# Optimization experiments

Measured on AMD Instinct MI355X. Metric: run time of the kernel, lower is better.

The kernel has to match this reference:

```python
import jax, jax.numpy as jnp
import numpy as np

B, N, D, L, H, DH, M, FF = 4, 2048, 512, 6, 8, 64, 266, 2048
EPS_LN = 1e-5
KERNEL_EPS = 1e-4


def fixed_pos_emb(n, dim):
    # performer_pytorch FixedPositionalEmbedding: cat(sin, cos) over half-dims
    inv_freq = 1.0 / (10000.0 ** (jnp.arange(0, dim, 2, dtype=jnp.float32) / dim))
    t = jnp.arange(n, dtype=jnp.float32)
    s = jnp.einsum('i,j->ij', t, inv_freq)  # [n, dim//2]
    return jnp.concatenate([jnp.sin(s), jnp.cos(s)], axis=-1)  # [n, dim]


def layer_norm(x, g, b):
    mu = x.mean(-1, keepdims=True)
    var = ((x - mu) ** 2).mean(-1, keepdims=True)
    return (x - mu) * jax.lax.rsqrt(var + EPS_LN) * g + b


def rotate_every_two(t):
    t1 = t[..., ::2]
    t2 = t[..., 1::2]
    return jnp.stack([-t2, t1], axis=-1).reshape(t.shape)


def apply_rotary(q, k, sinu):
    # sinu: [n, DH] = cat(sin_half, cos_half); repeat each value twice (interleaved)
    half = sinu.shape[-1] // 2
    sin = jnp.repeat(sinu[:, :half], 2, axis=-1)  # [n, DH]
    cos = jnp.repeat(sinu[:, half:], 2, axis=-1)
    q = q * cos + rotate_every_two(q) * sin
    k = k * cos + rotate_every_two(k) * sin
    return q, k


def softmax_kernel(data, proj, is_query):
    # data: [B,H,N,DH], proj: [M,DH]
    d = data.shape[-1]
    data_normalizer = d ** -0.25
    ratio = proj.shape[0] ** -0.5
    data_dash = jnp.einsum('bhnd,md->bhnm', data * data_normalizer, proj)
    diag = (data ** 2).sum(-1) * 0.5 * (data_normalizer ** 2)  # [B,H,N]
    if is_query:
        m = jnp.max(data_dash, axis=-1, keepdims=True)
    else:
        m = jnp.max(data_dash)
    return ratio * (jnp.exp(data_dash - diag[..., None] - m) + KERNEL_EPS)


def linear_attention(qf, kf, v):
    # qf/kf: [B,H,N,M], v: [B,H,N,DH]  (non-causal FAVOR+)
    k_sum = kf.sum(axis=-2)  # [B,H,M]
    d_inv = 1.0 / jnp.einsum('bhnm,bhm->bhn', qf, k_sum)
    context = jnp.einsum('bhnm,bhne->bhme', kf, v)  # [B,H,M,DH]
    return jnp.einsum('bhme,bhnm,bhn->bhne', context, qf, d_inv)


def setup_inputs() -> dict:
    key = jax.random.key(0)
    ks = jax.random.split(key, 8)
    std = 0.02
    inp = {
        'x': jax.random.normal(ks[0], (B, N, D), jnp.float32),
        'Wq': jax.random.normal(ks[1], (L, D, H * DH), jnp.float32) * std,
        'Wk': jax.random.normal(ks[2], (L, D, H * DH), jnp.float32) * std,
        'Wv': jax.random.normal(ks[3], (L, D, H * DH), jnp.float32) * std,
        'Wo': jax.random.normal(ks[4], (L, H * DH, D), jnp.float32) * std,
        'proj': jax.random.normal(ks[5], (L, M, DH), jnp.float32),
        'ln1_g': jnp.ones((L, D), jnp.float32),
        'ln1_b': jnp.zeros((L, D), jnp.float32),
        'W1': jax.random.normal(ks[6], (L, D, FF), jnp.float32) * std,
        'b1': jnp.zeros((L, FF), jnp.float32),
        'W2': jax.random.normal(ks[7], (L, FF, D), jnp.float32) * std,
        'b2': jnp.zeros((L, D), jnp.float32),
        'ln2_g': jnp.ones((L, D), jnp.float32),
        'ln2_b': jnp.zeros((L, D), jnp.float32),
        'lnf_g': jnp.ones((D,), jnp.float32),
        'lnf_b': jnp.zeros((D,), jnp.float32),
    }
    return inp


def reference(x, Wq, Wk, Wv, Wo, proj, ln1_g, ln1_b, W1, b1, W2, b2, ln2_g, ln2_b, lnf_g, lnf_b):
    n = x.shape[1]
    x = x + fixed_pos_emb(n, D)[None]          # additive sinusoidal emb
    sinu = fixed_pos_emb(n, DH)                 # per-head rotary table [n, DH]
    for i in range(L):
        # --- PreLayerNorm FAVOR+ self-attention ---
        h = layer_norm(x, ln1_g[i], ln1_b[i])
        q = jnp.einsum('bnd,de->bne', h, Wq[i]).reshape(B, n, H, DH).transpose(0, 2, 1, 3)
        k = jnp.einsum('bnd,de->bne', h, Wk[i]).reshape(B, n, H, DH).transpose(0, 2, 1, 3)
        v = jnp.einsum('bnd,de->bne', h, Wv[i]).reshape(B, n, H, DH).transpose(0, 2, 1, 3)
        q, k = apply_rotary(q, k, sinu)
        qf = softmax_kernel(q, proj[i], True)
        kf = softmax_kernel(k, proj[i], False)
        o = linear_attention(qf, kf, v)         # [B,H,n,DH]
        o = o.transpose(0, 2, 1, 3).reshape(B, n, H * DH)
        x = x + jnp.einsum('bne,ed->bnd', o, Wo[i])
        # --- PreLayerNorm FFN (GELU) ---
        h = layer_norm(x, ln2_g[i], ln2_b[i])
        h = jax.nn.gelu(jnp.einsum('bnd,df->bnf', h, W1[i]) + b1[i], approximate=False)
        x = x + jnp.einsum('bnf,fd->bnd', h, W2[i]) + b2[i]
    return layer_norm(x, lnf_g, lnf_b)
```

## Files before the change

kernel.cpp:

```cpp
#include <hip/hip_runtime.h>
#include <hip/hip_bf16.h>
#include <cstdint>

typedef float v4f __attribute__((ext_vector_type(4)));
typedef short v8s __attribute__((ext_vector_type(8)));
typedef unsigned short u16;

#define N_SEQ 2048
#define D_MODEL 512
#define N_LAYER 6
#define N_HEAD 8
#define D_HEAD 64
#define M_FEAT 266
#define M_PAD 288
#define M_ALLOC 384
#define FF_DIM 2048
#define BATCH 4
#define ROWS 8192
#define BHN 65536

__device__ __forceinline__ float b2f(u16 u) {
  return __uint_as_float(((uint32_t)u) << 16);
}
__device__ __forceinline__ u16 f2b(float f) {
  union { __hip_bfloat16 h; u16 u; } c;
  c.h = __float2bfloat16(f);
  return c.u;
}
__device__ __forceinline__ float wave_sum(float v) {
#pragma unroll
  for (int o = 1; o < 64; o <<= 1) v += __shfl_xor(v, o);
  return v;
}
__device__ __forceinline__ float wave_max(float v) {
#pragma unroll
  for (int o = 1; o < 64; o <<= 1) v = fmaxf(v, __shfl_xor(v, o));
  return v;
}

__device__ __forceinline__ float gelu_f(float x) {
  float ax = fabsf(x) * 0.70710678118f;
  float tt = __builtin_amdgcn_rcpf(fmaf(0.3275911f, ax, 1.0f));
  float poly = tt * fmaf(tt, fmaf(tt, fmaf(tt, fmaf(tt, 1.061405429f, -1.453152027f),
                                           1.421413741f), -0.284496736f), 0.254829592f);
  float er = 1.0f - poly * __expf(-ax * ax);
  er = copysignf(er, x);
  return 0.5f * x * (1.0f + er);
}

__device__ __forceinline__ void mfma_bf16(v4f& d, v8s a, v8s b) {
  asm volatile("v_mfma_f32_16x16x32_bf16 %0, %1, %2, %0" : "+v"(d) : "v"(a), "v"(b));
}

__device__ __forceinline__ void async16(const u16* g, u16* l) {
  __builtin_amdgcn_global_load_lds(
      (const __attribute__((address_space(1))) uint32_t*)g,
      (__attribute__((address_space(3))) uint32_t*)l, 16, 0, 0);
}

template <int EPI, int KSPLIT>
__global__ void __launch_bounds__(512, 2)
gemm3s(const u16* __restrict__ A, const u16* __restrict__ B,
       void* __restrict__ Cv, const float* __restrict__ bias,
       int K, int ldc)
{
  extern __shared__ u16 lds[];
  const int t = threadIdx.x;
  const int lane = t & 63;
  const int w = t >> 6;
  const int wm = w >> 2;
  const int wn = w & 3;
  const int tiM = blockIdx.x << 7, tiN = blockIdx.y << 8;
  const int ks = (KSPLIT > 1) ? blockIdx.z : 0;
  const int kchunk = K / KSPLIT;
  const int NT = kchunk >> 6;

  const int rr = lane & 15;
  const int kq = (lane >> 4) << 3;
  const int swz = (rr & 7) << 3;
  const int c0 = kq ^ swz;
  const int c1 = (32 + kq) ^ swz;

  const int prow = t >> 3;
  const int scol = (((t & 7) ^ (prow & 7)) << 3);
  const u16* Abase = A + (long long)(tiM + prow) * K + scol + (long long)ks * kchunk;
  const u16* Bbase = B + (long long)(tiN + prow) * K + scol + (long long)ks * kchunk;
  const long long r64 = 64LL * K;

  v4f acc[4][4] = {};

  auto stage6 = [&](int s, int kt) {
    const u16* sa = Abase + (long long)kt * 64;
    u16* da = &lds[s * 24576 + t * 8];
    async16(sa, da);
    async16(sa + r64, da + 4096);
    const u16* sb = Bbase + (long long)kt * 64;
    u16* db = &lds[s * 24576 + 8192 + t * 8];
#pragma unroll
    for (int j = 0; j < 4; j++) async16(sb + (long long)j * r64, db + j * 4096);
  };

  stage6(0, 0);
  stage6(1, 1);
  asm volatile("s_waitcnt vmcnt(6)" ::: "memory");
  __builtin_amdgcn_s_barrier();

  for (int kt = 0; kt < NT; ++kt) {
    const int s = kt % 3;
    const int sp = (kt + 2) % 3;
    const bool st = (kt + 2 < NT);
    const int ab = s * 24576;
    const int bb = ab + 8192;
    v8s a0[4], a1[4], b0[4], b1[4];
#pragma unroll
    for (int i = 0; i < 4; i++) {
      a0[i] = *(const v8s*)&lds[ab + (wm * 64 + i * 16 + rr) * 64 + c0];
      a1[i] = *(const v8s*)&lds[ab + (wm * 64 + i * 16 + rr) * 64 + c1];
      b0[i] = *(const v8s*)&lds[bb + (wn * 64 + i * 16 + rr) * 64 + c0];
      b1[i] = *(const v8s*)&lds[bb + (wn * 64 + i * 16 + rr) * 64 + c1];
    }
    if (st) stage6(sp, kt + 2);
    __builtin_amdgcn_s_setprio(1);
#pragma unroll
    for (int m = 0; m < 4; m++)
#pragma unroll
      for (int n = 0; n < 4; n++) {
        mfma_bf16(acc[m][n], a0[m], b0[n]);
        mfma_bf16(acc[m][n], a1[m], b1[n]);
      }
    __builtin_amdgcn_s_setprio(0);
    if (st) asm volatile("s_waitcnt vmcnt(6)" ::: "memory");
    else    asm volatile("s_waitcnt vmcnt(0)" ::: "memory");
    __builtin_amdgcn_s_barrier();
  }

  __builtin_amdgcn_sched_barrier(0);
  asm volatile("s_nop 7\ns_nop 7\ns_nop 7");
  __builtin_amdgcn_sched_barrier(0);

  const int r4 = (lane >> 4) << 2;
  const int cc = lane & 15;
#pragma unroll
  for (int mf = 0; mf < 4; mf++)
#pragma unroll
    for (int nf = 0; nf < 4; nf++)
#pragma unroll
      for (int i = 0; i < 4; i++) {
        int row = tiM + wm * 64 + mf * 16 + r4 + i;
        int col = tiN + wn * 64 + nf * 16 + cc;
        float v = acc[mf][nf][i];
        if (EPI == 0) {
          ((u16*)Cv)[(long long)row * ldc + col] = f2b(v);
        } else if (EPI == 3) {
          ((u16*)Cv)[(long long)row * ldc + col] = f2b(gelu_f(v + bias[col]));
        } else {
          ((float*)Cv)[((long long)ks * ROWS + row) * ldc + col] = v;
        }
      }
}

__global__ void ff2red(const float* __restrict__ part, const float* __restrict__ bias,
                       float* __restrict__ x)
{
  long long i = ((long long)blockIdx.x * 256 + threadIdx.x) * 8;
  int col = (int)(i & 511);
  v4f s0 = {}, s1 = {};
#pragma unroll
  for (int ks = 0; ks < 2; ks++) {
    const float* p = part + (long long)ks * (ROWS * 512LL) + i;
    s0 += *(const v4f*)p;
    s1 += *(const v4f*)(p + 4);
  }
  v4f b0 = *(const v4f*)(bias + col);
  v4f b1 = *(const v4f*)(bias + col + 4);
  v4f x0 = *(const v4f*)(x + i), x1 = *(const v4f*)(x + i + 4);
  x0 += s0 + b0;
  x1 += s1 + b1;
  *(v4f*)(x + i) = x0;
  *(v4f*)(x + i + 4) = x1;
}

template <int EPI, int BN, int KSPLIT>
__global__ void __launch_bounds__(256, 4)
gemm2(const u16* __restrict__ A, const u16* __restrict__ B,
      void* __restrict__ Cv, const float* __restrict__ bias,
      int K, int ldc, long long sA, long long sB, long long sC,
      float scale, int Ncap, int Mcap, unsigned int* __restrict__ gmax)
{
  __shared__ u16 As[2][128 * 32];
  __shared__ u16 Bs[2][BN * 32];
  __shared__ float smax[4];
  const int zz = blockIdx.z;
  const int z = (KSPLIT > 1) ? zz / KSPLIT : zz;
  const int ks = (KSPLIT > 1) ? zz % KSPLIT : 0;
  const int kchunk = K / KSPLIT;
  const u16* Ag = A + (long long)z * sA + ks * kchunk;
  const u16* Bg = B + (long long)z * sB + ks * kchunk;
  const int t = threadIdx.x;
  const int lane = t & 63;
  const int w = t >> 6;
  constexpr int NF = BN / 32;
  const int wm = (w >> 1) << 6;
  const int wn = (w & 1) * (BN / 2);
  const int tiM = blockIdx.x << 7, tiN = blockIdx.y * BN;

  const int srow = t >> 2;
  const int scol = (t & 3) << 3;
  const u16* Ap = Ag + (long long)(tiM + srow) * K + scol;
  const u16* Bp = Bg + (long long)(tiN + srow) * K + scol;
  const long long rstride = 64LL * K;

  const int rr = lane & 15;
  const int kc = (lane >> 4) << 3;

  v4f acc[4][NF] = {};

  const int nk = kchunk >> 5;
  auto stage = [&](int buf, int k0) {
    async16(Ap + k0, &As[buf][t * 8]);
    async16(Ap + k0 + rstride, &As[buf][t * 8 + 2048]);
    async16(Bp + k0, &Bs[buf][t * 8]);
    if (BN == 128) async16(Bp + k0 + rstride, &Bs[buf][t * 8 + 2048]);
  };

  stage(0, 0);
  __syncthreads();
  int cur = 0;
  for (int kt = 0; kt < nk; ++kt) {
    if (kt + 1 < nk) stage(cur ^ 1, (kt + 1) << 5);
    v8s af[4], bf[NF];
#pragma unroll
    for (int i = 0; i < 4; i++) af[i] = *(const v8s*)&As[cur][(wm + rr + i * 16) * 32 + kc];
#pragma unroll
    for (int i = 0; i < NF; i++) bf[i] = *(const v8s*)&Bs[cur][(wn + rr + i * 16) * 32 + kc];
#pragma unroll
    for (int fm = 0; fm < 4; fm++)
#pragma unroll
      for (int fn = 0; fn < NF; fn++)
        mfma_bf16(acc[fm][fn], af[fm], bf[fn]);
    __syncthreads();
    cur ^= 1;
  }

  __builtin_amdgcn_sched_barrier(0);
  asm volatile("s_nop 7\ns_nop 7\ns_nop 7");
  __builtin_amdgcn_sched_barrier(0);

  const int r4 = (lane >> 4) << 2;
  const int cc = lane & 15;
  float lmax = -3e38f;
#pragma unroll
  for (int fm = 0; fm < 4; fm++)
#pragma unroll
    for (int fn = 0; fn < NF; fn++)
#pragma unroll
      for (int i = 0; i < 4; i++) {
        int row = tiM + wm + fm * 16 + r4 + i;
        int col = tiN + wn + fn * 16 + cc;
        float v = acc[fm][fn][i];
        if (EPI == 5) {
          if (row < Mcap && col < Ncap)
            ((float*)Cv)[((long long)zz * M_ALLOC + row) * 64 + col] = v;
        } else if (EPI == 6) {
          float sv = v * scale;
          if (col < Ncap) ((float*)Cv)[(long long)row * ldc + col] = sv;
          if (col < M_FEAT) lmax = fmaxf(lmax, sv);
        }
      }

  if (EPI == 6) {
    lmax = wave_max(lmax);
    if (lane == 0) smax[w] = lmax;
    __syncthreads();
    if (t == 0) {
      float m = fmaxf(fmaxf(smax[0], smax[1]), fmaxf(smax[2], smax[3]));
      unsigned int u = __float_as_uint(m);
      unsigned int key = (u & 0x80000000u) ? ~u : (u | 0x80000000u);
      atomicMax(gmax, key);
    }
  }
}

template <int EPI>
__global__ void __launch_bounds__(256, 6)
gemm_small(const u16* __restrict__ A, const u16* __restrict__ B,
           void* __restrict__ Cv, const float* __restrict__ bias,
           int K, int ldc, long long sA, long long sB)
{
  __shared__ u16 As[2][64 * 32];
  __shared__ u16 Bs[2][64 * 32];
  const int z = blockIdx.z;
  const u16* Ag = A + (long long)z * sA;
  const u16* Bg = B + (long long)z * sB;
  const int t = threadIdx.x;
  const int lane = t & 63;
  const int w = t >> 6;
  const int wm = (w >> 1) << 5;
  const int wn = (w & 1) << 5;
  const int tiM = blockIdx.x << 6, tiN = blockIdx.y << 6;

  const int srow = t >> 2;
  const int scol = (t & 3) << 3;
  const u16* Ap = Ag + (long long)(tiM + srow) * K + scol;
  const u16* Bp = Bg + (long long)(tiN + srow) * K + scol;

  const int rr = lane & 15;
  const int kc = (lane >> 4) << 3;

  v4f acc[2][2] = {};

  const int nk = K >> 5;
  auto stage = [&](int buf, int k0) {
    async16(Ap + k0, &As[buf][t * 8]);
    async16(Bp + k0, &Bs[buf][t * 8]);
  };

  stage(0, 0);
  __syncthreads();
  int cur = 0;
  for (int kt = 0; kt < nk; ++kt) {
    if (kt + 1 < nk) stage(cur ^ 1, (kt + 1) << 5);
    v8s af[2], bf[2];
#pragma unroll
    for (int i = 0; i < 2; i++) af[i] = *(const v8s*)&As[cur][(wm + rr + i * 16) * 32 + kc];
#pragma unroll
    for (int i = 0; i < 2; i++) bf[i] = *(const v8s*)&Bs[cur][(wn + rr + i * 16) * 32 + kc];
#pragma unroll
    for (int fm = 0; fm < 2; fm++)
#pragma unroll
      for (int fn = 0; fn < 2; fn++)
        mfma_bf16(acc[fm][fn], af[fm], bf[fn]);
    __syncthreads();
    cur ^= 1;
  }

  __builtin_amdgcn_sched_barrier(0);
  asm volatile("s_nop 7\ns_nop 7\ns_nop 7");
  __builtin_amdgcn_sched_barrier(0);

  const int r4 = (lane >> 4) << 2;
  const int cc = lane & 15;
#pragma unroll
  for (int fm = 0; fm < 2; fm++)
#pragma unroll
    for (int fn = 0; fn < 2; fn++)
#pragma unroll
      for (int i = 0; i < 4; i++) {
        int row = tiM + wm + fm * 16 + r4 + i;
        int col = tiN + wn + fn * 16 + cc;
        float v = acc[fm][fn][i];
        if (EPI == 0) {
          ((u16*)Cv)[(long long)row * ldc + col] = f2b(v);
        } else if (EPI == 2) {
          long long idx = (long long)row * ldc + col;
          float bb = bias ? bias[col] : 0.0f;
          ((float*)Cv)[idx] += v + bb;
        } else if (EPI == 3) {
          ((u16*)Cv)[(long long)row * ldc + col] = f2b(gelu_f(v + bias[col]));
        } else {
          int b_ = z >> 3, h_ = z & 7;
          ((u16*)Cv)[(long long)(b_ * N_SEQ + row) * 512 + h_ * 64 + col] = f2b(v);
        }
      }
}

__global__ void __launch_bounds__(384, 3)
ddq_qf(const u16* __restrict__ qr, const u16* __restrict__ proj,
       const float* __restrict__ diag, const float* __restrict__ ksum,
       u16* __restrict__ qf)
{
  __shared__ u16 As[2][64 * 32];
  __shared__ u16 Bs[2][288 * 32];
  __shared__ float redw[6][64];
  __shared__ float rowv[64];
  __shared__ float sdg[64];
  const int bh = blockIdx.z;
  const int tiM = blockIdx.x << 6;
  const int t = threadIdx.x;
  const int lane = t & 63;
  const int w = t >> 6;
  const u16* Ag = qr + (long long)bh * (N_SEQ * 64);
  const int srow = t >> 2, scol = (t & 3) << 3;
  const u16* Ap = Ag + (long long)(tiM + srow) * 64 + scol;
  const int rr = lane & 15, kc = (lane >> 4) << 3;
  const int wn = w * 48;

  if (t < 64) sdg[t] = diag[(long long)bh * N_SEQ + tiM + t];

  v4f acc[4][3] = {};
  auto stage = [&](int buf, int k0) {
    if (t < 256) async16(Ap + k0, &As[buf][t * 8]);
#pragma unroll
    for (int j = 0; j < 3; j++) {
      int idx = j * 384 + t;
      async16(proj + (long long)(idx >> 2) * 64 + ((idx & 3) << 3) + k0,
              &Bs[buf][j * 3072 + t * 8]);
    }
  };

  stage(0, 0);
  __syncthreads();
  for (int kt = 0; kt < 2; ++kt) {
    if (kt == 0) stage(1, 32);
    v8s af[4], bf[3];
#pragma unroll
    for (int i = 0; i < 4; i++) af[i] = *(const v8s*)&As[kt][(rr + i * 16) * 32 + kc];
#pragma unroll
    for (int i = 0; i < 3; i++) bf[i] = *(const v8s*)&Bs[kt][(wn + i * 16 + rr) * 32 + kc];
#pragma unroll
    for (int fm = 0; fm < 4; fm++)
#pragma unroll
      for (int fn = 0; fn < 3; fn++)
        mfma_bf16(acc[fm][fn], af[fm], bf[fn]);
    __syncthreads();
  }

  __builtin_amdgcn_sched_barrier(0);
  asm volatile("s_nop 7\ns_nop 7\ns_nop 7");
  __builtin_amdgcn_sched_barrier(0);

  const int r4 = (lane >> 4) << 2;
  const int cc = lane & 15;
  const float sc = 0.35355339f;

#pragma unroll
  for (int fm = 0; fm < 4; fm++)
#pragma unroll
    for (int i = 0; i < 4; i++) {
      float m = -3e38f;
#pragma unroll
      for (int fn = 0; fn < 3; fn++) {
        int col = wn + fn * 16 + cc;
        float v = acc[fm][fn][i] * sc;
        if (col < M_FEAT) m = fmaxf(m, v);
      }
#pragma unroll
      for (int o = 1; o < 16; o <<= 1) m = fmaxf(m, __shfl_xor(m, o));
      if (cc == 0) redw[w][fm * 16 + r4 + i] = m;
    }
  __syncthreads();
  if (t < 64) {
    float g = redw[0][t];
#pragma unroll
    for (int ww = 1; ww < 6; ww++) g = fmaxf(g, redw[ww][t]);
    rowv[t] = g;
  }
  __syncthreads();

  float ksv[3];
#pragma unroll
  for (int fn = 0; fn < 3; fn++) ksv[fn] = ksum[bh * M_PAD + wn + fn * 16 + cc];

#pragma unroll
  for (int fm = 0; fm < 4; fm++)
#pragma unroll
    for (int i = 0; i < 4; i++) {
      int row = fm * 16 + r4 + i;
      float gm = rowv[row];
      float dg = sdg[row];
      float s = 0.0f;
#pragma unroll
      for (int fn = 0; fn < 3; fn++) {
        float e = 0.06131389f * (expf(acc[fm][fn][i] * sc - dg - gm) + 1e-4f);
        acc[fm][fn][i] = e;
        s += e * ksv[fn];
      }
#pragma unroll
      for (int o = 1; o < 16; o <<= 1) s += __shfl_xor(s, o);
      if (cc == 0) redw[w][row] = s;
    }
  __syncthreads();
  if (t < 64) {
    float s = redw[0][t];
#pragma unroll
    for (int ww = 1; ww < 6; ww++) s += redw[ww][t];
    rowv[t] = 1.0f / s;
  }
  __syncthreads();

#pragma unroll
  for (int fm = 0; fm < 4; fm++)
#pragma unroll
    for (int i = 0; i < 4; i++) {
      int row = fm * 16 + r4 + i;
      float dinv = rowv[row];
#pragma unroll
      for (int fn = 0; fn < 3; fn++) {
        int col = wn + fn * 16 + cc;
        qf[((long long)bh * N_SEQ + tiM + row) * M_PAD + col] =
            f2b(acc[fm][fn][i] * dinv);
      }
    }
}

template <bool F32OUT>
__global__ void ln_kernel(const float* __restrict__ x, const float* __restrict__ g,
                          const float* __restrict__ b, void* __restrict__ out)
{
  const int row = blockIdx.x * 4 + (threadIdx.x >> 6);
  const int lane = threadIdx.x & 63;
  const float* xr = x + (long long)row * D_MODEL + lane * 8;
  v4f v0 = *(const v4f*)xr;
  v4f v1 = *(const v4f*)(xr + 4);
  float s = v0[0] + v0[1] + v0[2] + v0[3] + v1[0] + v1[1] + v1[2] + v1[3];
  float sq = v0[0]*v0[0] + v0[1]*v0[1] + v0[2]*v0[2] + v0[3]*v0[3]
           + v1[0]*v1[0] + v1[1]*v1[1] + v1[2]*v1[2] + v1[3]*v1[3];
  s = wave_sum(s);
  sq = wave_sum(sq);
  float mu = s * (1.0f / D_MODEL);
  float var = sq * (1.0f / D_MODEL) - mu * mu;
  float rstd = rsqrtf(var + 1e-5f);
  v4f g0 = *(const v4f*)(g + lane * 8), g1 = *(const v4f*)(g + lane * 8 + 4);
  v4f bb0 = *(const v4f*)(b + lane * 8), bb1 = *(const v4f*)(b + lane * 8 + 4);
  float y[8];
#pragma unroll
  for (int j = 0; j < 4; j++) y[j] = (v0[j] - mu) * rstd * g0[j] + bb0[j];
#pragma unroll
  for (int j = 0; j < 4; j++) y[4 + j] = (v1[j] - mu) * rstd * g1[j] + bb1[j];
  if (F32OUT) {
    float* op = (float*)out + (long long)row * D_MODEL + lane * 8;
    v4f o0 = {y[0], y[1], y[2], y[3]}, o1 = {y[4], y[5], y[6], y[7]};
    *(v4f*)op = o0;
    *(v4f*)(op + 4) = o1;
  } else {
    u16* op = (u16*)out + (long long)row * D_MODEL + lane * 8;
    alignas(16) u16 tmp[8];
#pragma unroll
    for (int j = 0; j < 8; j++) tmp[j] = f2b(y[j]);
    *(v8s*)op = *(v8s*)tmp;
  }
}

__global__ void posadd(const float* __restrict__ xin, float* __restrict__ x)
{
  long long i = (long long)blockIdx.x * 256 + threadIdx.x;
  int d = (int)(i & 511);
  int n = (int)((i >> 9) & 2047);
  int j = d & 255;
  float sarg = (float)n * expf(-0.035977892f * (float)j);
  float pe = (d < 256) ? sinf(sarg) : cosf(sarg);
  x[i] = xin[i] + pe;
}

__global__ void rotab(float* __restrict__ ts, float* __restrict__ tc)
{
  int i = blockIdx.x * 64 + threadIdx.x;
  int n = i >> 5, j = i & 31;
  float sarg = (float)n * expf(-0.28782314f * (float)j);
  float s, c;
  sincosf(sarg, &s, &c);
  ts[i] = s;
  tc[i] = c;
}

__global__ void rotary_kernel(const u16* __restrict__ qkv,
                              const float* __restrict__ ts, const float* __restrict__ tc,
                              u16* __restrict__ qr, u16* __restrict__ kr,
                              float* __restrict__ dq, float* __restrict__ dk)
{
  int bid = blockIdx.x * 4 + (threadIdx.x >> 6);
  int n = bid & 2047;
  int h = (bid >> 11) & 7;
  int b = bid >> 14;
  int lane = threadIdx.x & 63;
  long long src = ((long long)(b * N_SEQ + n)) * 1536 + h * 64 + lane;
  float qv = b2f(qkv[src]);
  float kv = b2f(qkv[src + 512]);
  int j = lane >> 1;
  float sn = ts[n * 32 + j], cn = tc[n * 32 + j];
  float qp = __shfl_xor(qv, 1), kp = __shfl_xor(kv, 1);
  float qrv = (lane & 1) ? (qv * cn + qp * sn) : (qv * cn - qp * sn);
  float krv = (lane & 1) ? (kv * cn + kp * sn) : (kv * cn - kp * sn);
  u16 qb = f2b(qrv), kb = f2b(krv);
  long long dst = ((long long)bid) * 64 + lane;
  qr[dst] = qb;
  kr[dst] = kb;
  float q2 = b2f(qb); q2 *= q2;
  float k2 = b2f(kb); k2 *= k2;
  q2 = wave_sum(q2);
  k2 = wave_sum(k2);
  if (lane == 0) { dq[bid] = q2 * 0.0625f; dk[bid] = k2 * 0.0625f; }
}

__global__ void vtrans(const u16* __restrict__ qkv, u16* __restrict__ vT)
{
  int bid = blockIdx.x;
  int nt = bid & 31;
  int h = (bid >> 5) & 7;
  int b = bid >> 8;
  __shared__ u16 st[64][72];
  int t = threadIdx.x;
  int r = t >> 2, c = (t & 3) << 4;
  long long src = ((long long)(b * N_SEQ + nt * 64 + r)) * 1536 + 1024 + h * 64 + c;
  *(v8s*)&st[r][c] = *(const v8s*)(qkv + src);
  *(v8s*)&st[r][c + 8] = *(const v8s*)(qkv + src + 8);
  __syncthreads();
  alignas(16) u16 tmp[16];
#pragma unroll
  for (int jj = 0; jj < 16; jj++) tmp[jj] = st[c + jj][r];
  long long dst = ((long long)((b * 8 + h) * 64 + r)) * N_SEQ + nt * 64 + c;
  *(v8s*)(vT + dst) = *(v8s*)&tmp[0];
  *(v8s*)(vT + dst + 8) = *(v8s*)&tmp[8];
}

__global__ void wtrans(const float* __restrict__ src, u16* __restrict__ dst,
                       int Ks, int Ns, long long sSrc, long long sDst)
{
  int l = blockIdx.z;
  src += (long long)l * sSrc;
  dst += (long long)l * sDst;
  int n0 = blockIdx.x << 6, k0 = blockIdx.y << 6;
  __shared__ float st[64][68];
  int t = threadIdx.x;
  int r = t >> 2, c = (t & 3) << 4;
  const float* sp = src + (long long)(k0 + r) * Ns + n0 + c;
#pragma unroll
  for (int jj = 0; jj < 16; jj += 4) *(v4f*)&st[r][c + jj] = *(const v4f*)(sp + jj);
  __syncthreads();
  alignas(16) u16 tmp[16];
#pragma unroll
  for (int jj = 0; jj < 16; jj++) tmp[jj] = f2b(st[c + jj][r]);
  u16* dp = dst + (long long)(n0 + r) * Ks + k0 + c;
  *(v8s*)(dp) = *(v8s*)&tmp[0];
  *(v8s*)(dp + 8) = *(v8s*)&tmp[8];
}

__global__ void projconv(const float* __restrict__ proj, u16* __restrict__ out)
{
  int i = blockIdx.x * 256 + threadIdx.x;
  int dh = i & 63;
  int m = (i >> 6) % M_ALLOC;
  int l = i / (M_ALLOC * 64);
  float v = (m < M_FEAT) ? proj[((long long)l * M_FEAT + m) * 64 + dh] : 0.0f;
  out[i] = f2b(v);
}

__global__ void resetmax(unsigned int* p) { *p = 0u; }

__global__ void kfprep(const float* __restrict__ dd, const float* __restrict__ diag,
                       const unsigned int* __restrict__ kmax,
                       u16* __restrict__ kfT, float* __restrict__ part)
{
  int ntile = blockIdx.x;
  int m0 = blockIdx.y << 6;
  int bh = blockIdx.z;
  int n0 = ntile << 6;
  __shared__ float st[64][65];
  unsigned int kk = kmax[0];
  float km = (kk & 0x80000000u) ? __uint_as_float(kk ^ 0x80000000u)
                                : __uint_as_float(~kk);
  int t = threadIdx.x;
  int r = t >> 2, c = (t & 3) << 4;
  const float* dp = dd + ((long long)bh * N_SEQ + n0 + r) * M_PAD + m0 + c;
  float dg = diag[(long long)bh * N_SEQ + n0 + r];
  float vals[16];
  if (m0 + c + 16 <= M_PAD) {
#pragma unroll
    for (int j = 0; j < 16; j += 4) *(v4f*)&vals[j] = *(const v4f*)(dp + j);
  } else {
#pragma unroll
    for (int j = 0; j < 16; j++) vals[j] = (m0 + c + j < M_PAD) ? dp[j] : 0.0f;
  }
#pragma unroll
  for (int j = 0; j < 16; j++) {
    int m = m0 + c + j;
    float e = (m < M_FEAT) ? 0.06131389f * (expf(vals[j] - dg - km) + 1e-4f) : 0.0f;
    st[r][c + j] = e;
  }
  __syncthreads();
  int mr = t >> 2, nc = (t & 3) << 4;
  float s = 0.0f;
  alignas(16) u16 tmp[16];
#pragma unroll
  for (int j = 0; j < 16; j++) {
    float e = st[nc + j][mr];
    s += e;
    tmp[j] = f2b(e);
  }
  s += __shfl_xor(s, 1);
  s += __shfl_xor(s, 2);
  int m = m0 + mr;
  if (m < M_PAD) {
    u16* op = kfT + ((long long)bh * M_ALLOC + m) * N_SEQ + n0 + nc;
    *(v8s*)op = *(v8s*)&tmp[0];
    *(v8s*)(op + 8) = *(v8s*)&tmp[8];
    if ((t & 3) == 0)
      part[((long long)bh * M_PAD + m) * 32 + ntile] = s;
  }
}

__global__ void ksumred(const float* __restrict__ part, float* __restrict__ ksum)
{
  int i = blockIdx.x * 256 + threadIdx.x;
  if (i >= 32 * M_PAD) return;
  const float* p = part + (long long)i * 32;
  float s = 0.0f;
#pragma unroll
  for (int j = 0; j < 32; j += 4) {
    v4f v = *(const v4f*)(p + j);
    s += v[0] + v[1] + v[2] + v[3];
  }
  ksum[i] = s;
}

__global__ void ctxred(const float* __restrict__ part, u16* __restrict__ ctxT)
{
  int bh = blockIdx.y;
  int m0 = blockIdx.x << 6;
  __shared__ float st[64][65];
  int t = threadIdx.x;
  int r = t >> 2, c = (t & 3) << 4;
  int m = m0 + r;
  v4f s[4] = {};
  if (m < M_PAD) {
    for (int ks = 0; ks < 8; ks++) {
      const float* p = part + (((long long)bh * 8 + ks) * M_ALLOC + m) * 64 + c;
#pragma unroll
      for (int j = 0; j < 4; j++) s[j] += *(const v4f*)(p + j * 4);
    }
  }
#pragma unroll
  for (int j = 0; j < 4; j++)
#pragma unroll
    for (int e = 0; e < 4; e++) st[r][c + j * 4 + e] = s[j][e];
  __syncthreads();
  int e = t >> 2, mc = (t & 3) << 4;
  if (m0 + mc < M_PAD) {
    alignas(16) u16 tmp[16];
#pragma unroll
    for (int j = 0; j < 16; j++) tmp[j] = f2b(st[mc + j][e]);
    u16* op = ctxT + ((long long)bh * 64 + e) * M_PAD + m0 + mc;
    *(v8s*)op = *(v8s*)&tmp[0];
    *(v8s*)(op + 8) = *(v8s*)&tmp[8];
  }
}

extern "C" void kernel_launch(void* const* d_in, const int* in_sizes, int n_in,
                              void* d_out, int out_size, void* d_ws, size_t ws_size,
                              hipStream_t stream)
{
  const float* x_in = (const float*)d_in[0];
  const float* Wq  = (const float*)d_in[1];
  const float* Wk  = (const float*)d_in[2];
  const float* Wv  = (const float*)d_in[3];
  const float* Wo  = (const float*)d_in[4];
  const float* Pr  = (const float*)d_in[5];
  const float* ln1g = (const float*)d_in[6];
  const float* ln1b = (const float*)d_in[7];
  const float* W1  = (const float*)d_in[8];
  const float* b1  = (const float*)d_in[9];
  const float* W2  = (const float*)d_in[10];
  const float* b2  = (const float*)d_in[11];
  const float* ln2g = (const float*)d_in[12];
  const float* ln2b = (const float*)d_in[13];
  const float* lnfg = (const float*)d_in[14];
  const float* lnfb = (const float*)d_in[15];

  hipFuncSetAttribute(reinterpret_cast<const void*>(&gemm3s<0, 1>),
                      hipFuncAttributeMaxDynamicSharedMemorySize, 147456);
  hipFuncSetAttribute(reinterpret_cast<const void*>(&gemm3s<3, 1>),
                      hipFuncAttributeMaxDynamicSharedMemorySize, 147456);
  hipFuncSetAttribute(reinterpret_cast<const void*>(&gemm3s<5, 2>),
                      hipFuncAttributeMaxDynamicSharedMemorySize, 147456);

  char* ws = (char*)d_ws;
  size_t off = 0;
  auto alloc = [&](size_t bytes) -> void* {
    void* p = ws + off;
    off = (off + bytes + 255) & ~(size_t)255;
    return p;
  };

  float* x      = (float*)alloc((size_t)ROWS * D_MODEL * 4);
  float* tsin   = (float*)alloc((size_t)N_SEQ * 32 * 4);
  float* tcos   = (float*)alloc((size_t)N_SEQ * 32 * 4);
  u16*   wqkvT  = (u16*)alloc((size_t)N_LAYER * 1536 * 512 * 2);
  u16*   woT    = (u16*)alloc((size_t)N_LAYER * 512 * 512 * 2);
  u16*   w1T    = (u16*)alloc((size_t)N_LAYER * 2048 * 512 * 2);
  u16*   w2T    = (u16*)alloc((size_t)N_LAYER * 512 * 2048 * 2);
  u16*   projT  = (u16*)alloc((size_t)N_LAYER * M_ALLOC * 64 * 2);
  u16*   hbuf   = (u16*)alloc((size_t)ROWS * D_MODEL * 2);
  u16*   obuf   = (u16*)alloc((size_t)ROWS * D_MODEL * 2);
  float* big    = (float*)alloc((size_t)32 * N_SEQ * M_PAD * 4);
  u16*   qrbuf  = (u16*)alloc((size_t)BHN * 64 * 2);
  u16*   krbuf  = (u16*)alloc((size_t)BHN * 64 * 2);
  u16*   vTbuf  = (u16*)alloc((size_t)BHN * 64 * 2);
  float* diagq  = (float*)alloc((size_t)BHN * 4);
  float* diagk  = (float*)alloc((size_t)BHN * 4);
  unsigned int* kmaxu = (unsigned int*)alloc(256);
  u16*   kfT    = (u16*)alloc((size_t)32 * M_ALLOC * N_SEQ * 2);
  float* part   = (float*)alloc((size_t)32 * 8 * M_ALLOC * 64 * 4);
  float* kspart = (float*)alloc((size_t)32 * M_PAD * 32 * 4);
  u16*   ctxT   = (u16*)alloc((size_t)32 * 64 * M_PAD * 2);
  float* ksum   = (float*)alloc((size_t)32 * M_PAD * 4);
  (void)alloc(1 << 20);
  (void)ws_size; (void)in_sizes; (void)n_in; (void)out_size;
  float* ff2part = (float*)kfT;

  posadd<<<16384, 256, 0, stream>>>(x_in, x);
  rotab<<<1024, 64, 0, stream>>>(tsin, tcos);
  wtrans<<<dim3(8, 8, 6), 256, 0, stream>>>(Wq, wqkvT, 512, 512, 512LL * 512, 1536LL * 512);
  wtrans<<<dim3(8, 8, 6), 256, 0, stream>>>(Wk, wqkvT + 512LL * 512, 512, 512, 512LL * 512, 1536LL * 512);
  wtrans<<<dim3(8, 8, 6), 256, 0, stream>>>(Wv, wqkvT + 1024LL * 512, 512, 512, 512LL * 512, 1536LL * 512);
  wtrans<<<dim3(8, 8, 6), 256, 0, stream>>>(Wo, woT, 512, 512, 512LL * 512, 512LL * 512);
  wtrans<<<dim3(32, 8, 6), 256, 0, stream>>>(W1, w1T, 512, 2048, 512LL * 2048, 2048LL * 512);
  wtrans<<<dim3(8, 32, 6), 256, 0, stream>>>(W2, w2T, 2048, 512, 2048LL * 512, 512LL * 2048);
  projconv<<<(N_LAYER * M_ALLOC * 64) / 256, 256, 0, stream>>>(Pr, projT);

  for (int l = 0; l < N_LAYER; l++) {
    const u16* wq = wqkvT + (long long)l * 1536 * 512;
    const u16* wo = woT + (long long)l * 512 * 512;
    const u16* w1 = w1T + (long long)l * 2048 * 512;
    const u16* w2 = w2T + (long long)l * 512 * 2048;
    const u16* pj = projT + (long long)l * M_ALLOC * 64;

    resetmax<<<1, 1, 0, stream>>>(kmaxu);
    ln_kernel<false><<<ROWS / 4, 256, 0, stream>>>(x, ln1g + l * 512, ln1b + l * 512, hbuf);
    gemm3s<0, 1><<<dim3(64, 6), 512, 147456, stream>>>(hbuf, wq, big, nullptr, 512, 1536);
    rotary_kernel<<<BHN / 4, 256, 0, stream>>>((u16*)big, tsin, tcos, qrbuf, krbuf, diagq, diagk);
    vtrans<<<1024, 256, 0, stream>>>((u16*)big, vTbuf);
    gemm2<6, 128, 1><<<dim3(512, 3, 1), 256, 0, stream>>>(krbuf, pj, big, nullptr,
        64, M_PAD, 0, 0, 0, 0.35355339f, M_PAD, BHN, kmaxu);
    kfprep<<<dim3(32, 5, 32), 256, 0, stream>>>(big, diagk, kmaxu, kfT, kspart);
    ksumred<<<(32 * M_PAD + 255) / 256, 256, 0, stream>>>(kspart, ksum);
    gemm2<5, 64, 8><<<dim3(3, 1, 256), 256, 0, stream>>>(kfT, vTbuf, part, nullptr,
        2048, 64, (long long)M_ALLOC * N_SEQ, 64LL * N_SEQ, 0, 1.0f, 64, M_PAD, nullptr);
    ctxred<<<dim3(5, 32), 256, 0, stream>>>(part, ctxT);
    ddq_qf<<<dim3(32, 1, 32), 384, 0, stream>>>(qrbuf, pj, diagq, ksum, kfT);
    gemm_small<4><<<dim3(32, 1, 32), 256, 0, stream>>>(kfT, ctxT, obuf, nullptr,
        M_PAD, 0, (long long)N_SEQ * M_PAD, 64LL * M_PAD);
    gemm_small<2><<<dim3(128, 8, 1), 256, 0, stream>>>(obuf, wo, x, nullptr,
        512, 512, 0, 0);
    ln_kernel<false><<<ROWS / 4, 256, 0, stream>>>(x, ln2g + l * 512, ln2b + l * 512, hbuf);
    gemm3s<3, 1><<<dim3(64, 8), 512, 147456, stream>>>(hbuf, w1, big, b1 + (long long)l * 2048,
        512, 2048);
    gemm3s<5, 2><<<dim3(64, 2, 2), 512, 147456, stream>>>((u16*)big, w2, ff2part, nullptr,
        2048, 512);
    ff2red<<<2048, 256, 0, stream>>>(ff2part, b2 + (long long)l * 512, x);
  }

  ln_kernel<true><<<ROWS / 4, 256, 0, stream>>>(x, lnfg, lnfb, d_out);
}
```

Measured before the change: 1.526 ms.

## Halve gemm3s K-tile to raise occupancy and split FF2 four ways

The main bf16 GEMM now stages 32-wide K tiles instead of 64-wide, using a new LDS swizzle and three async loads per stage. This halves dynamic shared memory to 72 KB and lets launch bounds ask for four blocks per CU instead of two. The FF2 GEMM moves from a 2-way to a 4-way K split to launch more blocks, and its reduction kernel now sums four partials. The cost is twice as many barrier-synchronised iterations, tighter register limits, and more partial-sum traffic through ff2part, which must be large enough to hold four partials.

```diff
diff --git a/kernel.cpp b/kernel.cpp
--- a/kernel.cpp
+++ b/kernel.cpp
@@ -59,7 +59,7 @@
 }
 
 template <int EPI, int KSPLIT>
-__global__ void __launch_bounds__(512, 2)
+__global__ void __launch_bounds__(512, 4)
 gemm3s(const u16* __restrict__ A, const u16* __restrict__ B,
        void* __restrict__ Cv, const float* __restrict__ bias,
        int K, int ldc)
@@ -73,63 +73,54 @@
   const int tiM = blockIdx.x << 7, tiN = blockIdx.y << 8;
   const int ks = (KSPLIT > 1) ? blockIdx.z : 0;
   const int kchunk = K / KSPLIT;
-  const int NT = kchunk >> 6;
+  const int NT = kchunk >> 5;
 
   const int rr = lane & 15;
   const int kq = (lane >> 4) << 3;
-  const int swz = (rr & 7) << 3;
-  const int c0 = kq ^ swz;
-  const int c1 = (32 + kq) ^ swz;
-
-  const int prow = t >> 3;
-  const int scol = (((t & 7) ^ (prow & 7)) << 3);
-  const u16* Abase = A + (long long)(tiM + prow) * K + scol + (long long)ks * kchunk;
-  const u16* Bbase = B + (long long)(tiN + prow) * K + scol + (long long)ks * kchunk;
-  const long long r64 = 64LL * K;
+  const int sw = ((rr >> 1) & 3) << 3;
+  const int cr = kq ^ sw;
+
+  const int srow = t >> 2;
+  const int scol = (((t & 3) ^ ((srow >> 1) & 3)) << 3);
+  const u16* Abase = A + (long long)(tiM + srow) * K + scol + (long long)ks * kchunk;
+  const u16* Bbase = B + (long long)(tiN + srow) * K + scol + (long long)ks * kchunk;
+  const long long r128 = 128LL * K;
 
   v4f acc[4][4] = {};
 
-  auto stage6 = [&](int s, int kt) {
-    const u16* sa = Abase + (long long)kt * 64;
-    u16* da = &lds[s * 24576 + t * 8];
-    async16(sa, da);
-    async16(sa + r64, da + 4096);
-    const u16* sb = Bbase + (long long)kt * 64;
-    u16* db = &lds[s * 24576 + 8192 + t * 8];
-#pragma unroll
-    for (int j = 0; j < 4; j++) async16(sb + (long long)j * r64, db + j * 4096);
+  auto stage3 = [&](int s, int kt) {
+    const long long k0 = (long long)kt * 32;
+    u16* d = &lds[s * 12288 + t * 8];
+    async16(Abase + k0, d);
+    async16(Bbase + k0, d + 4096);
+    async16(Bbase + k0 + r128, d + 8192);
   };
 
-  stage6(0, 0);
-  stage6(1, 1);
-  asm volatile("s_waitcnt vmcnt(6)" ::: "memory");
+  stage3(0, 0);
+  stage3(1, 1);
+  asm volatile("s_waitcnt vmcnt(3)" ::: "memory");
   __builtin_amdgcn_s_barrier();
 
   for (int kt = 0; kt < NT; ++kt) {
     const int s = kt % 3;
     const int sp = (kt + 2) % 3;
     const bool st = (kt + 2 < NT);
-    const int ab = s * 24576;
-    const int bb = ab + 8192;
-    v8s a0[4], a1[4], b0[4], b1[4];
+    const int ab = s * 12288;
+    const int bb = ab + 4096;
+    v8s af[4], bf[4];
 #pragma unroll
     for (int i = 0; i < 4; i++) {
-      a0[i] = *(const v8s*)&lds[ab + (wm * 64 + i * 16 + rr) * 64 + c0];
-      a1[i] = *(const v8s*)&lds[ab + (wm * 64 + i * 16 + rr) * 64 + c1];
-      b0[i] = *(const v8s*)&lds[bb + (wn * 64 + i * 16 + rr) * 64 + c0];
-      b1[i] = *(const v8s*)&lds[bb + (wn * 64 + i * 16 + rr) * 64 + c1];
+      af[i] = *(const v8s*)&lds[ab + (wm * 64 + i * 16 + rr) * 32 + cr];
+      bf[i] = *(const v8s*)&lds[bb + (wn * 64 + i * 16 + rr) * 32 + cr];
     }
-    if (st) stage6(sp, kt + 2);
+    if (st) stage3(sp, kt + 2);
     __builtin_amdgcn_s_setprio(1);
 #pragma unroll
     for (int m = 0; m < 4; m++)
 #pragma unroll
-      for (int n = 0; n < 4; n++) {
-        mfma_bf16(acc[m][n], a0[m], b0[n]);
-        mfma_bf16(acc[m][n], a1[m], b1[n]);
-      }
+      for (int n = 0; n < 4; n++) mfma_bf16(acc[m][n], af[m], bf[n]);
     __builtin_amdgcn_s_setprio(0);
-    if (st) asm volatile("s_waitcnt vmcnt(6)" ::: "memory");
+    if (st) asm volatile("s_waitcnt vmcnt(3)" ::: "memory");
     else    asm volatile("s_waitcnt vmcnt(0)" ::: "memory");
     __builtin_amdgcn_s_barrier();
   }
@@ -166,7 +157,7 @@
   int col = (int)(i & 511);
   v4f s0 = {}, s1 = {};
 #pragma unroll
-  for (int ks = 0; ks < 2; ks++) {
+  for (int ks = 0; ks < 4; ks++) {
     const float* p = part + (long long)ks * (ROWS * 512LL) + i;
     s0 += *(const v4f*)p;
     s1 += *(const v4f*)(p + 4);
@@ -757,11 +748,11 @@
   const float* lnfb = (const float*)d_in[15];
 
   hipFuncSetAttribute(reinterpret_cast<const void*>(&gemm3s<0, 1>),
-                      hipFuncAttributeMaxDynamicSharedMemorySize, 147456);
+                      hipFuncAttributeMaxDynamicSharedMemorySize, 73728);
   hipFuncSetAttribute(reinterpret_cast<const void*>(&gemm3s<3, 1>),
-                      hipFuncAttributeMaxDynamicSharedMemorySize, 147456);
-  hipFuncSetAttribute(reinterpret_cast<const void*>(&gemm3s<5, 2>),
-                      hipFuncAttributeMaxDynamicSharedMemorySize, 147456);
+                      hipFuncAttributeMaxDynamicSharedMemorySize, 73728);
+  hipFuncSetAttribute(reinterpret_cast<const void*>(&gemm3s<5, 4>),
+                      hipFuncAttributeMaxDynamicSharedMemorySize, 73728);
 
   char* ws = (char*)d_ws;
   size_t off = 0;
@@ -816,7 +807,7 @@
 
     resetmax<<<1, 1, 0, stream>>>(kmaxu);
     ln_kernel<false><<<ROWS / 4, 256, 0, stream>>>(x, ln1g + l * 512, ln1b + l * 512, hbuf);
-    gemm3s<0, 1><<<dim3(64, 6), 512, 147456, stream>>>(hbuf, wq, big, nullptr, 512, 1536);
+    gemm3s<0, 1><<<dim3(64, 6), 512, 73728, stream>>>(hbuf, wq, big, nullptr, 512, 1536);
     rotary_kernel<<<BHN / 4, 256, 0, stream>>>((u16*)big, tsin, tcos, qrbuf, krbuf, diagq, diagk);
     vtrans<<<1024, 256, 0, stream>>>((u16*)big, vTbuf);
     gemm2<6, 128, 1><<<dim3(512, 3, 1), 256, 0, stream>>>(krbuf, pj, big, nullptr,
@@ -832,9 +823,9 @@
     gemm_small<2><<<dim3(128, 8, 1), 256, 0, stream>>>(obuf, wo, x, nullptr,
         512, 512, 0, 0);
     ln_kernel<false><<<ROWS / 4, 256, 0, stream>>>(x, ln2g + l * 512, ln2b + l * 512, hbuf);
-    gemm3s<3, 1><<<dim3(64, 8), 512, 147456, stream>>>(hbuf, w1, big, b1 + (long long)l * 2048,
+    gemm3s<3, 1><<<dim3(64, 8), 512, 73728, stream>>>(hbuf, w1, big, b1 + (long long)l * 2048,
         512, 2048);
-    gemm3s<5, 2><<<dim3(64, 2, 2), 512, 147456, stream>>>((u16*)big, w2, ff2part, nullptr,
+    gemm3s<5, 4><<<dim3(64, 2, 4), 512, 73728, stream>>>((u16*)big, w2, ff2part, nullptr,
         2048, 512);
     ff2red<<<2048, 256, 0, stream>>>(ff2part, b2 + (long long)l * 512, x);
   }
```

Result: no change. 1.549 ms (+1.5%).
